# Kernel tuning notes

Measured on AMD Instinct MI355X. Metric: run time of the kernel, lower is better.

Reference implementation:

```python
import jax, jax.numpy as jnp
import numpy as np

B, P, L1, D = 64, 16, 16, 1024  # images, people/img, object slots/img (slot0=no-object), feat dim
SP = 32   # flattened spatial (Conv_spatial output channels)
PROJ = 512
ACT = 29


def setup_inputs() -> dict:
    key = jax.random.key(0)
    ks = jax.random.split(key, 16)
    rn = lambda k, s, sc=1.0: jax.random.normal(k, s, dtype=jnp.float32) * sc
    w = 0.02  # weight init scale
    return {
        "people": rn(ks[0], (B, P, D)),
        "objects": rn(ks[1], (B, L1, D)),
        "context": rn(ks[2], (B, D)),
        "spatial": rn(ks[3], (B, P * L1, SP)),
        "Wvis_w": rn(ks[4], (3 * D, PROJ), w), "Wvis_b": jnp.zeros((PROJ,), jnp.float32),
        "Wspat_w": rn(ks[5], (SP, PROJ), w), "Wspat_b": jnp.zeros((PROJ,), jnp.float32),
        "Wip_w": rn(ks[6], (PROJ, 1), w), "Wip_b": jnp.zeros((1,), jnp.float32),
        "Wref_w": rn(ks[7], (PROJ, ACT), w), "Wref_b": jnp.zeros((ACT,), jnp.float32),
        "Watt_w": rn(ks[8], (PROJ, ACT), w), "Watt_b": jnp.zeros((ACT,), jnp.float32),
        "Woh_w": rn(ks[9], (D, D), w), "Woh_b": jnp.zeros((D,), jnp.float32),
        "Who_w": rn(ks[10], (D, D), w), "Who_b": jnp.zeros((D,), jnp.float32),
        "Wg_w": rn(ks[11], (2 * D, ACT), w), "Wg_b": jnp.zeros((ACT,), jnp.float32),
    }


def reference(people, objects, context, spatial,
              Wvis_w, Wvis_b, Wspat_w, Wspat_b, Wip_w, Wip_b,
              Wref_w, Wref_b, Watt_w, Watt_b,
              Woh_w, Woh_b, Who_w, Who_b, Wg_w, Wg_b):
    Bn, Pn, Dn = people.shape
    L = objects.shape[1]
    C = Bn * Pn * L

    # --- ROI.pairing: all (person, object-slot) pairs + image context -> [C, 3D]
    pe = jnp.broadcast_to(people[:, :, None, :], (Bn, Pn, L, Dn))
    ob = jnp.broadcast_to(objects[:, None, :, :], (Bn, Pn, L, Dn))
    cx = jnp.broadcast_to(context[:, None, None, :], (Bn, Pn, L, Dn))
    pairs = jnp.concatenate([pe, ob, cx], axis=-1).reshape(C, 3 * Dn)

    # --- attention / visual projection heads
    a_ho = jax.nn.relu(spatial.reshape(C, -1) @ Wspat_w + Wspat_b)   # W_Spat
    f_vis = jax.nn.relu(pairs @ Wvis_w + Wvis_b)                     # W_vis
    f_ref = f_vis * a_ho
    i_ho = f_ref @ Wip_w + Wip_b                                     # [C,1]
    interaction_prob = jax.nn.sigmoid(i_ho)
    p_ref = f_ref @ Wref_w + Wref_b                                  # [C,29]
    p_att = a_ho @ Watt_w + Watt_b                                   # [C,29]

    # --- graph message passing: adjacency = interaction probs, skipping slot 0 (no-object)
    adj = interaction_prob.reshape(Bn, Pn, L)[:, :, 1:]              # [B,P,O]
    oh = jax.nn.relu(objects[:, 1:] @ Woh_w + Woh_b)                 # W_oh on objects
    ho = jax.nn.relu(people @ Who_w + Who_b)                         # W_ho on people
    people_r = people + jnp.einsum('bpo,bod->bpd', adj, oh)
    objects_r = objects[:, 1:] + jnp.einsum('bpo,bpd->bod', adj, ho)
    objects_full = jnp.concatenate([objects[:, :1], objects_r], axis=1)  # re-attach no-object slot

    # --- refined all-pairs concat -> W_graph
    pe_r = jnp.broadcast_to(people_r[:, :, None, :], (Bn, Pn, L, Dn))
    ob_r = jnp.broadcast_to(objects_full[:, None, :, :], (Bn, Pn, L, Dn))
    pairs_g = jnp.concatenate([pe_r, ob_r], axis=-1).reshape(C, 2 * Dn)
    p_graph = pairs_g @ Wg_w + Wg_b                                  # [C,29]

    return (i_ho, p_ref, p_att, p_graph)
```

## Files before the change

kernel.cpp:

```cpp
#include <hip/hip_runtime.h>


typedef unsigned short u16;
typedef short s16x8 __attribute__((ext_vector_type(8)));
typedef float f32x4 __attribute__((ext_vector_type(4)));

__device__ __forceinline__ u16 f2b(float f) {
    union { float f; unsigned int i; } v; v.f = f;
    unsigned int r = (v.i + 0x7fffu + ((v.i >> 16) & 1u)) >> 16;
    return (u16)r;
}
__device__ __forceinline__ float b2f(u16 u) {
    union { float f; unsigned int i; } v; v.i = ((unsigned int)u) << 16; return v.f;
}
__device__ __forceinline__ unsigned int pack2(float x, float y) {
    return (unsigned int)f2b(x) | ((unsigned int)f2b(y) << 16);
}

#define OFF_WSPATT 0u
#define OFF_WREFT  32768u
#define OFF_WATTT  65536u
#define OFF_WGT    98304u
#define OFF_PP     229376u
#define OFF_PO     1277952u
#define OFF_PC     2326528u
#define OFF_ADJ    2392064u
#define OFF_HP     2457600u
#define OFF_HOF    2588672u
#define OFF_YH     2719744u
#define OFF_ZO     2850816u
#define ZERO_OFF   2457600u
#define ZERO_LEN   516096u
#define OFF_WVIST2 2973696u
#define OFF_WHOT2  6119424u
#define OFF_WOHT2  8216576u
#define OFF_PEOB   10313728u
#define OFF_OBJB   12410880u
#define OFF_CTXB   14508032u
#define OFF_SPATB  14639104u

__global__ __launch_bounds__(256) void prep_all(
    const float* __restrict__ people, const float* __restrict__ objects,
    const float* __restrict__ context, const float* __restrict__ spatial,
    const float* __restrict__ Wvis, const float* __restrict__ Who,
    const float* __restrict__ Woh, const float* __restrict__ Wspat,
    const float* __restrict__ Wref, const float* __restrict__ Watt,
    const float* __restrict__ Wg,
    u16* __restrict__ peoB, u16* __restrict__ objB, u16* __restrict__ ctxB,
    u16* __restrict__ spatB, u16* __restrict__ WvisT, u16* __restrict__ WhoT,
    u16* __restrict__ WohT, u16* __restrict__ WspatT, u16* __restrict__ WrefT,
    u16* __restrict__ WattT, u16* __restrict__ WgT, float* __restrict__ zeroWS)
{
    __shared__ float S[64][65];
    int bid = blockIdx.x, t = threadIdx.x;
    if (bid < 896) {
        const float* src; u16* dst; int N, K, kt, nt;
        int tb = bid;
        if (tb < 256)      { src = Who;  dst = WhoT;  K = 1024; N = 1024; kt = tb >> 4; nt = tb & 15; }
        else if (tb < 512) { tb -= 256; src = Woh;  dst = WohT;  K = 1024; N = 1024; kt = tb >> 4; nt = tb & 15; }
        else               { tb -= 512; src = Wvis; dst = WvisT; K = 3072; N = 512;  kt = tb >> 3; nt = tb & 7; }
        int k0 = kt * 64, n0 = nt * 64;
        int r = t >> 4, c4 = (t & 15) * 4;
#pragma unroll
        for (int i = 0; i < 4; i++) {
            float4 v = *(const float4*)&src[(size_t)(k0 + r + 16 * i) * N + n0 + c4];
            S[r + 16 * i][c4 + 0] = v.x;
            S[r + 16 * i][c4 + 1] = v.y;
            S[r + 16 * i][c4 + 2] = v.z;
            S[r + 16 * i][c4 + 3] = v.w;
        }
        __syncthreads();
#pragma unroll
        for (int i = 0; i < 4; i++) {
            int nn = r + 16 * i;
            unsigned int lo = pack2(S[c4 + 0][nn], S[c4 + 1][nn]);
            unsigned int hi = pack2(S[c4 + 2][nn], S[c4 + 3][nn]);
            *(uint2*)&dst[(size_t)(n0 + nn) * K + k0 + c4] = make_uint2(lo, hi);
        }
        return;
    }
    int g = (bid - 896) * 256 + t;
    const int gsz = 512 * 256;
    for (int i = g; i < 262144; i += gsz) {
        float4 v = ((const float4*)people)[i];
        ((uint2*)peoB)[i] = make_uint2(pack2(v.x, v.y), pack2(v.z, v.w));
    }
    for (int i = g; i < 262144; i += gsz) {
        float4 v = ((const float4*)objects)[i];
        ((uint2*)objB)[i] = make_uint2(pack2(v.x, v.y), pack2(v.z, v.w));
    }
    for (int i = g; i < 16384; i += gsz) {
        float4 v = ((const float4*)context)[i];
        ((uint2*)ctxB)[i] = make_uint2(pack2(v.x, v.y), pack2(v.z, v.w));
    }
    for (int i = g; i < 131072; i += gsz) {
        float4 v = ((const float4*)spatial)[i];
        ((uint2*)spatB)[i] = make_uint2(pack2(v.x, v.y), pack2(v.z, v.w));
    }
    for (int i = g; i < 32256; i += gsz) {
        f32x4 z = {0.f, 0.f, 0.f, 0.f};
        ((f32x4*)zeroWS)[i] = z;
    }
    for (int i = g; i < 512 * 32; i += gsz) {
        int n = i >> 5, k = i & 31;
        WspatT[i] = f2b(Wspat[k * 512 + n]);
    }
    for (int i = g; i < 32 * 512; i += gsz) {
        int n = i >> 9, k = i & 511;
        WrefT[i] = (n < 29) ? f2b(Wref[k * 29 + n]) : (u16)0;
        WattT[i] = (n < 29) ? f2b(Watt[k * 29 + n]) : (u16)0;
    }
    for (int i = g; i < 32 * 2048; i += gsz) {
        int n = i >> 11, k = i & 2047;
        WgT[i] = (n < 29) ? f2b(Wg[k * 29 + n]) : (u16)0;
    }
}

__global__ __launch_bounds__(256) void fused_gemms(
    const u16* __restrict__ peoB, const u16* __restrict__ objB,
    const u16* __restrict__ ctxB, const u16* __restrict__ WvisT,
    const u16* __restrict__ WhoT, const float* __restrict__ Who_b,
    const u16* __restrict__ WohT, const float* __restrict__ Woh_b,
    const u16* __restrict__ WgT,
    u16* __restrict__ Pp, u16* __restrict__ Po, u16* __restrict__ Pc,
    float* __restrict__ Yh, float* __restrict__ Zo,
    float* __restrict__ Hp, float* __restrict__ HoF)
{
    __shared__ __align__(16) u16 As[2][64][72];
    __shared__ __align__(16) u16 Bs[2][64][72];

    int b0 = blockIdx.x, bid;
    if (b0 < 264)      bid = (b0 & 7) * 33 + (b0 >> 3);
    else if (b0 < 760) { int l = b0 - 264; bid = 264 + (l & 7) * 62 + (l >> 3); }
    else               { int l = b0 - 760; bid = 760 + (l & 7) * 16 + (l >> 3); }
    int t = threadIdx.x;
    int lane = t & 63, w = t >> 6;
    int l16 = lane & 15, q = lane >> 4;
    int wy = w >> 1, wx = w & 1;

    if (bid < 760) {
        const u16 *Ap, *Bp;
        int Bstride, bm, bn, koff = 0, zrm = 0;
        u16* outB = nullptr;
        const float* bb = nullptr; const u16* Wg2 = nullptr; float* U = nullptr;
        if (bid < 264) {
            int bx = bid & 7, ty = bid >> 3;
            if (ty < 16)      { Ap = peoB; outB = Pp; koff = 0;    bm = ty * 64; }
            else if (ty < 32) { Ap = objB; outB = Po; koff = 1024; bm = (ty - 16) * 64; }
            else              { Ap = ctxB; outB = Pc; koff = 2048; bm = 0; }
            bn = bx * 64;
            Bp = WvisT; Bstride = 3072;
        } else {
            int r3 = bid - 264;
            int zz, rt, nbt;
            if (r3 < 256) { zz = 0; rt = r3 >> 4; nbt = r3 & 15; }
            else          { zz = 1; r3 -= 256; rt = r3 >> 4; nbt = r3 & 15; }
            zrm = zz;
            Ap = zz ? objB : peoB;
            Bp = zz ? WohT : WhoT; Bstride = 1024;
            bb = zz ? Woh_b : Who_b;
            Wg2 = zz ? WgT : WgT + 1024;
            U = zz ? Zo : Yh;
            bm = rt * 64; bn = nbt * 64;
        }

        int tr = t >> 3, tc = (t & 7) * 8;
        int a0r = bm + tr, a1r = bm + 32 + tr;
        if (zrm) { a0r = (a0r / 15) * 16 + (a0r % 15) + 1;
                   a1r = (a1r / 15) * 16 + (a1r % 15) + 1; }
        const u16* gA0 = Ap + (size_t)a0r * 1024 + tc;
        const u16* gA1 = Ap + (size_t)a1r * 1024 + tc;
        const u16* gB0 = Bp + (size_t)(bn + tr) * Bstride + koff + tc;
        const u16* gB1 = Bp + (size_t)(bn + 32 + tr) * Bstride + koff + tc;

        s16x8 rA0 = *(const s16x8*)gA0, rA1 = *(const s16x8*)gA1;
        s16x8 rB0 = *(const s16x8*)gB0, rB1 = *(const s16x8*)gB1;
        gA0 += 64; gA1 += 64; gB0 += 64; gB1 += 64;
        *(s16x8*)&As[0][tr][tc]      = rA0;
        *(s16x8*)&As[0][32 + tr][tc] = rA1;
        *(s16x8*)&Bs[0][tr][tc]      = rB0;
        *(s16x8*)&Bs[0][32 + tr][tc] = rB1;
        rA0 = *(const s16x8*)gA0; rA1 = *(const s16x8*)gA1;
        rB0 = *(const s16x8*)gB0; rB1 = *(const s16x8*)gB1;
        gA0 += 64; gA1 += 64; gB0 += 64; gB1 += 64;
        __syncthreads();

        f32x4 acc00 = {0,0,0,0}, acc01 = {0,0,0,0}, acc10 = {0,0,0,0}, acc11 = {0,0,0,0};
        int cur = 0;
        for (int kt = 0; kt < 16; kt++) {
#pragma unroll
            for (int kk = 0; kk < 2; kk++) {
                s16x8 a0 = *(const s16x8*)&As[cur][wy * 32 + l16][kk * 32 + q * 8];
                s16x8 a1 = *(const s16x8*)&As[cur][wy * 32 + 16 + l16][kk * 32 + q * 8];
                s16x8 b0 = *(const s16x8*)&Bs[cur][wx * 32 + l16][kk * 32 + q * 8];
                s16x8 b1 = *(const s16x8*)&Bs[cur][wx * 32 + 16 + l16][kk * 32 + q * 8];
                acc00 = __builtin_amdgcn_mfma_f32_16x16x32_bf16(a0, b0, acc00, 0, 0, 0);
                acc01 = __builtin_amdgcn_mfma_f32_16x16x32_bf16(a0, b1, acc01, 0, 0, 0);
                acc10 = __builtin_amdgcn_mfma_f32_16x16x32_bf16(a1, b0, acc10, 0, 0, 0);
                acc11 = __builtin_amdgcn_mfma_f32_16x16x32_bf16(a1, b1, acc11, 0, 0, 0);
            }
            if (kt < 15) {
                __syncthreads();
                *(s16x8*)&As[cur ^ 1][tr][tc]      = rA0;
                *(s16x8*)&As[cur ^ 1][32 + tr][tc] = rA1;
                *(s16x8*)&Bs[cur ^ 1][tr][tc]      = rB0;
                *(s16x8*)&Bs[cur ^ 1][32 + tr][tc] = rB1;
                if (kt < 14) {
                    rA0 = *(const s16x8*)gA0; rA1 = *(const s16x8*)gA1;
                    rB0 = *(const s16x8*)gB0; rB1 = *(const s16x8*)gB1;
                    gA0 += 64; gA1 += 64; gB0 += 64; gB1 += 64;
                }
                __syncthreads();
                cur ^= 1;
            }
        }

        f32x4 accs[2][2] = {{acc00, acc01}, {acc10, acc11}};
        if (bid < 264) {
#pragma unroll
            for (int ii = 0; ii < 2; ii++)
#pragma unroll
                for (int jj = 0; jj < 2; jj++) {
                    int col = bn + wx * 32 + jj * 16 + l16;
#pragma unroll
                    for (int r = 0; r < 4; r++) {
                        int row = bm + wy * 32 + ii * 16 + q * 4 + r;
                        outB[(size_t)row * 512 + col] = f2b(accs[ii][jj][r]);
                    }
                }
        } else {
            u16 (*T)[72] = As[0];
#pragma unroll
            for (int ii = 0; ii < 2; ii++)
#pragma unroll
                for (int jj = 0; jj < 2; jj++) {
                    int col = wx * 32 + jj * 16 + l16;
                    float bv = bb[bn + col];
#pragma unroll
                    for (int rr = 0; rr < 4; rr++) {
                        float v = accs[ii][jj][rr] + bv;
                        T[wy * 32 + ii * 16 + q * 4 + rr][col] = f2b(fmaxf(v, 0.f));
                    }
                }
            __syncthreads();

            f32x4 s20 = {0,0,0,0}, s21 = {0,0,0,0};
#pragma unroll
            for (int kk = 0; kk < 64; kk += 32) {
                s16x8 a2 = *(const s16x8*)(&T[w * 16 + l16][kk + q * 8]);
                s16x8 b20 = *(const s16x8*)(Wg2 + (size_t)l16 * 2048 + bn + kk + q * 8);
                s16x8 b21 = *(const s16x8*)(Wg2 + (size_t)(16 + l16) * 2048 + bn + kk + q * 8);
                s20 = __builtin_amdgcn_mfma_f32_16x16x32_bf16(a2, b20, s20, 0, 0, 0);
                s21 = __builtin_amdgcn_mfma_f32_16x16x32_bf16(a2, b21, s21, 0, 0, 0);
            }
#pragma unroll
            for (int rr = 0; rr < 4; rr++) {
                int row = bm + w * 16 + q * 4 + rr;
                atomicAdd(&U[(size_t)row * 32 + l16], s20[rr]);
                atomicAdd(&U[(size_t)row * 32 + 16 + l16], s21[rr]);
            }
        }
    } else {
        int r3 = bid - 760;
        int bx = r3 & 7, by = (r3 >> 3) & 7, z = r3 >> 6;
        const u16* A  = z ? objB : peoB;
        const u16* BT = z ? WgT + 1024 : WgT;
        float* outF   = z ? HoF : Hp;
        int bm = bx * 128 + w * 32;
        int kb = by * 128;
        const u16* ap0 = A + (size_t)(bm + l16) * 1024 + kb + q * 8;
        const u16* ap1 = A + (size_t)(bm + 16 + l16) * 1024 + kb + q * 8;
        const u16* bp0 = BT + (size_t)l16 * 2048 + kb + q * 8;
        const u16* bp1 = BT + (size_t)(16 + l16) * 2048 + kb + q * 8;
        f32x4 acc00 = {0,0,0,0}, acc01 = {0,0,0,0}, acc10 = {0,0,0,0}, acc11 = {0,0,0,0};
        s16x8 bA0[4], bA1[4], bB0[4], bB1[4];
#pragma unroll
        for (int s = 0; s < 4; s++) {
            bA0[s] = *(const s16x8*)(ap0 + s * 32);
            bA1[s] = *(const s16x8*)(ap1 + s * 32);
            bB0[s] = *(const s16x8*)(bp0 + s * 32);
            bB1[s] = *(const s16x8*)(bp1 + s * 32);
        }
#pragma unroll
        for (int s = 0; s < 4; s++) {
            acc00 = __builtin_amdgcn_mfma_f32_16x16x32_bf16(bA0[s], bB0[s], acc00, 0, 0, 0);
            acc01 = __builtin_amdgcn_mfma_f32_16x16x32_bf16(bA0[s], bB1[s], acc01, 0, 0, 0);
            acc10 = __builtin_amdgcn_mfma_f32_16x16x32_bf16(bA1[s], bB0[s], acc10, 0, 0, 0);
            acc11 = __builtin_amdgcn_mfma_f32_16x16x32_bf16(bA1[s], bB1[s], acc11, 0, 0, 0);
        }
        f32x4 accs[2][2] = {{acc00, acc01}, {acc10, acc11}};
#pragma unroll
        for (int ii = 0; ii < 2; ii++)
#pragma unroll
            for (int jj = 0; jj < 2; jj++)
#pragma unroll
                for (int r = 0; r < 4; r++)
                    atomicAdd(&outF[(size_t)(bm + ii * 16 + q * 4 + r) * 32 + jj * 16 + l16],
                              accs[ii][jj][r]);
    }
}

__global__ __launch_bounds__(256) void mega(
    const u16* __restrict__ spatB, const u16* __restrict__ WspatT,
    const float* __restrict__ bspat,
    const u16* __restrict__ Pp, const u16* __restrict__ Po,
    const u16* __restrict__ Pc, const float* __restrict__ bvis,
    const u16* __restrict__ WrefT, const float* __restrict__ bref,
    const u16* __restrict__ WattT, const float* __restrict__ batt,
    const float* __restrict__ wip, const float* __restrict__ bip,
    float* __restrict__ outI, float* __restrict__ outRef,
    float* __restrict__ outAtt, float* __restrict__ adjw)
{
    __shared__ u16 tile[32][512];
    __shared__ float part[32][8];
    __shared__ float wipS[512];
    int t = threadIdx.x;
    int b0 = blockIdx.x;
    int bid = (b0 & 7) * 64 + (b0 >> 3);
    int c0 = bid * 32;
    int lane = t & 63, w = t >> 6;
    int l16 = lane & 15, q = lane >> 4;

    {
        float2 u = *(const float2*)(wip + t * 2);
        wipS[t * 2]     = u.x;
        wipS[t * 2 + 1] = u.y;
    }

    {
        s16x8 a0 = *(const s16x8*)(spatB + (size_t)(c0 + l16) * 32 + q * 8);
        s16x8 a1 = *(const s16x8*)(spatB + (size_t)(c0 + 16 + l16) * 32 + q * 8);
        const u16* wb = WspatT + (size_t)(w * 128 + l16) * 32 + q * 8;
        s16x8 cb = *(const s16x8*)wb;
        s16x8 nb_ = *(const s16x8*)(wb + 16 * 32);
        wb += 32 * 32;
#pragma unroll
        for (int nt = 0; nt < 8; nt++) {
            s16x8 tb;
            if (nt < 6) { tb = *(const s16x8*)wb; wb += 16 * 32; }
            int n = w * 128 + nt * 16;
            f32x4 acc0 = {0,0,0,0}, acc1 = {0,0,0,0};
            acc0 = __builtin_amdgcn_mfma_f32_16x16x32_bf16(a0, cb, acc0, 0, 0, 0);
            acc1 = __builtin_amdgcn_mfma_f32_16x16x32_bf16(a1, cb, acc1, 0, 0, 0);
            cb = nb_; nb_ = tb;
            float bias = bspat[n + l16];
#pragma unroll
            for (int r = 0; r < 4; r++) {
                tile[q * 4 + r][n + l16]      = f2b(fmaxf(acc0[r] + bias, 0.f));
                tile[16 + q * 4 + r][n + l16] = f2b(fmaxf(acc1[r] + bias, 0.f));
            }
        }
    }
    __syncthreads();

    {
        int rt = w >> 1, ct = w & 1;
        const u16* bp = WattT + (size_t)(ct * 16 + l16) * 512 + q * 8;
        const u16* ar = &tile[rt * 16 + l16][q * 8];
        f32x4 acc0 = {0,0,0,0}, acc1 = {0,0,0,0}, acc2 = {0,0,0,0}, acc3 = {0,0,0,0};
#pragma unroll
        for (int s = 0; s < 16; s += 4) {
            s16x8 a0 = *(const s16x8*)(ar + (s + 0) * 32);
            s16x8 a1 = *(const s16x8*)(ar + (s + 1) * 32);
            s16x8 a2 = *(const s16x8*)(ar + (s + 2) * 32);
            s16x8 a3 = *(const s16x8*)(ar + (s + 3) * 32);
            s16x8 b0 = *(const s16x8*)(bp + (s + 0) * 32);
            s16x8 b1 = *(const s16x8*)(bp + (s + 1) * 32);
            s16x8 b2 = *(const s16x8*)(bp + (s + 2) * 32);
            s16x8 b3 = *(const s16x8*)(bp + (s + 3) * 32);
            acc0 = __builtin_amdgcn_mfma_f32_16x16x32_bf16(a0, b0, acc0, 0, 0, 0);
            acc1 = __builtin_amdgcn_mfma_f32_16x16x32_bf16(a1, b1, acc1, 0, 0, 0);
            acc2 = __builtin_amdgcn_mfma_f32_16x16x32_bf16(a2, b2, acc2, 0, 0, 0);
            acc3 = __builtin_amdgcn_mfma_f32_16x16x32_bf16(a3, b3, acc3, 0, 0, 0);
        }
        f32x4 acc = (acc0 + acc1) + (acc2 + acc3);
        int col = ct * 16 + l16;
        if (col < 29) {
            float bias = batt[col];
#pragma unroll
            for (int r = 0; r < 4; r++) {
                int row = c0 + rt * 16 + q * 4 + r;
                outAtt[(size_t)row * 29 + col] = acc[r] + bias;
            }
        }
    }
    __syncthreads();

    {
        int row = t >> 3, g = t & 7;
        int c = c0 + row;
        int rp = c >> 4, bimg = c >> 8;
        int ro = bimg * 16 + (c & 15);
        const u16* ppr = Pp + (size_t)rp * 512;
        const u16* por = Po + (size_t)ro * 512;
        const u16* pcr = Pc + (size_t)bimg * 512;
        float ps = 0.f;
#pragma unroll 4
        for (int j = 0; j < 64; j += 2) {
            int col = g * 64 + j;
            unsigned int upp = *(const unsigned int*)(ppr + col);
            unsigned int upo = *(const unsigned int*)(por + col);
            unsigned int upc = *(const unsigned int*)(pcr + col);
            float2 bv = *(const float2*)(bvis + col);
            unsigned int uah = *(const unsigned int*)(&tile[row][col]);
            float fv0 = fmaxf(b2f((u16)(upp & 0xffff)) + b2f((u16)(upo & 0xffff))
                            + b2f((u16)(upc & 0xffff)) + bv.x, 0.f);
            float fv1 = fmaxf(b2f((u16)(upp >> 16)) + b2f((u16)(upo >> 16))
                            + b2f((u16)(upc >> 16)) + bv.y, 0.f);
            float fr0 = fv0 * b2f((u16)(uah & 0xffff));
            float fr1 = fv1 * b2f((u16)(uah >> 16));
            *(unsigned int*)(&tile[row][col]) = pack2(fr0, fr1);
            ps += fr0 * wipS[col] + fr1 * wipS[col + 1];
        }
        part[row][g] = ps;
    }
    __syncthreads();

    if (t < 32) {
        float s = part[t][0] + part[t][1] + part[t][2] + part[t][3]
                + part[t][4] + part[t][5] + part[t][6] + part[t][7] + bip[0];
        outI[c0 + t] = s;
        adjw[c0 + t] = 1.f / (1.f + expf(-s));
    }

    {
        int rt = w >> 1, ct = w & 1;
        const u16* bp = WrefT + (size_t)(ct * 16 + l16) * 512 + q * 8;
        const u16* ar = &tile[rt * 16 + l16][q * 8];
        f32x4 acc0 = {0,0,0,0}, acc1 = {0,0,0,0}, acc2 = {0,0,0,0}, acc3 = {0,0,0,0};
#pragma unroll
        for (int s = 0; s < 16; s += 4) {
            s16x8 a0 = *(const s16x8*)(ar + (s + 0) * 32);
            s16x8 a1 = *(const s16x8*)(ar + (s + 1) * 32);
            s16x8 a2 = *(const s16x8*)(ar + (s + 2) * 32);
            s16x8 a3 = *(const s16x8*)(ar + (s + 3) * 32);
            s16x8 b0 = *(const s16x8*)(bp + (s + 0) * 32);
            s16x8 b1 = *(const s16x8*)(bp + (s + 1) * 32);
            s16x8 b2 = *(const s16x8*)(bp + (s + 2) * 32);
            s16x8 b3 = *(const s16x8*)(bp + (s + 3) * 32);
            acc0 = __builtin_amdgcn_mfma_f32_16x16x32_bf16(a0, b0, acc0, 0, 0, 0);
            acc1 = __builtin_amdgcn_mfma_f32_16x16x32_bf16(a1, b1, acc1, 0, 0, 0);
            acc2 = __builtin_amdgcn_mfma_f32_16x16x32_bf16(a2, b2, acc2, 0, 0, 0);
            acc3 = __builtin_amdgcn_mfma_f32_16x16x32_bf16(a3, b3, acc3, 0, 0, 0);
        }
        f32x4 acc = (acc0 + acc1) + (acc2 + acc3);
        int col = ct * 16 + l16;
        if (col < 29) {
            float bias = bref[col];
#pragma unroll
            for (int r = 0; r < 4; r++) {
                int row = c0 + rt * 16 + q * 4 + r;
                outRef[(size_t)row * 29 + col] = acc[r] + bias;
            }
        }
    }
}

__global__ __launch_bounds__(256) void pgraph2(
    const float* __restrict__ adjw, const float* __restrict__ Hp,
    const float* __restrict__ HoF, const float* __restrict__ Yh,
    const float* __restrict__ Zo, const float* __restrict__ bg,
    float* __restrict__ outG)
{
    int b = blockIdx.x, t = threadIdx.x;
    __shared__ float adjS[16][16];
    __shared__ float YhS[16][32];
    __shared__ float ZoS[15][32];
    __shared__ float PA[16][32];
    __shared__ float OA[16][32];
    adjS[t >> 4][t & 15] = adjw[b * 256 + t];
    for (int i = t; i < 512; i += 256)
        YhS[i >> 5][i & 31] = Yh[(size_t)(b * 16 + (i >> 5)) * 32 + (i & 31)];
    for (int i = t; i < 480; i += 256)
        ZoS[i >> 5][i & 31] = Zo[(size_t)(b * 15 + (i >> 5)) * 32 + (i & 31)];
    __syncthreads();
    for (int i = t; i < 512; i += 256) {
        int p = i >> 5, j = i & 31;
        float s = 0.f;
#pragma unroll
        for (int o = 0; o < 15; o++) s += adjS[p][o + 1] * ZoS[o][j];
        PA[p][j] = s;
        float s2 = 0.f;
#pragma unroll
        for (int pp = 0; pp < 16; pp++) s2 += adjS[pp][p] * YhS[pp][j];
        OA[p][j] = s2;
    }
    __syncthreads();
    int p = t >> 4, l = t & 15;
    const float* hp = Hp + (size_t)(b * 16 + p) * 32;
    const float* ho = HoF + (size_t)(b * 16 + l) * 32;
    size_t c = (size_t)b * 256 + t;
    for (int j = 0; j < 29; j++) {
        float v = hp[j] + ho[j] + bg[j] + PA[p][j];
        if (l >= 1) v += OA[l][j];
        outG[c * 29 + j] = v;
    }
}

extern "C" void kernel_launch(void* const* d_in, const int* in_sizes, int n_in,
                              void* d_out, int out_size, void* d_ws, size_t ws_size,
                              hipStream_t stream)
{
    const float* people  = (const float*)d_in[0];
    const float* objects = (const float*)d_in[1];
    const float* context = (const float*)d_in[2];
    const float* spatial = (const float*)d_in[3];
    const float* Wvis_w  = (const float*)d_in[4];
    const float* Wvis_b  = (const float*)d_in[5];
    const float* Wspat_w = (const float*)d_in[6];
    const float* Wspat_b = (const float*)d_in[7];
    const float* Wip_w   = (const float*)d_in[8];
    const float* Wip_b   = (const float*)d_in[9];
    const float* Wref_w  = (const float*)d_in[10];
    const float* Wref_b  = (const float*)d_in[11];
    const float* Watt_w  = (const float*)d_in[12];
    const float* Watt_b  = (const float*)d_in[13];
    const float* Woh_w   = (const float*)d_in[14];
    const float* Woh_b   = (const float*)d_in[15];
    const float* Who_w   = (const float*)d_in[16];
    const float* Who_b   = (const float*)d_in[17];
    const float* Wg_w    = (const float*)d_in[18];
    const float* Wg_b    = (const float*)d_in[19];

    char* ws = (char*)d_ws;
    u16* WspatT = (u16*)(ws + OFF_WSPATT);
    u16* WrefT  = (u16*)(ws + OFF_WREFT);
    u16* WattT  = (u16*)(ws + OFF_WATTT);
    u16* WgT    = (u16*)(ws + OFF_WGT);
    u16* Ppb    = (u16*)(ws + OFF_PP);
    u16* Pob    = (u16*)(ws + OFF_PO);
    u16* Pcb    = (u16*)(ws + OFF_PC);
    float* adjw = (float*)(ws + OFF_ADJ);
    float* Hp   = (float*)(ws + OFF_HP);
    float* HoF  = (float*)(ws + OFF_HOF);
    float* Yh   = (float*)(ws + OFF_YH);
    float* Zo   = (float*)(ws + OFF_ZO);
    u16* WvisT2 = (u16*)(ws + OFF_WVIST2);
    u16* WhoT2  = (u16*)(ws + OFF_WHOT2);
    u16* WohT2  = (u16*)(ws + OFF_WOHT2);
    u16* peoB   = (u16*)(ws + OFF_PEOB);
    u16* objB   = (u16*)(ws + OFF_OBJB);
    u16* ctxB   = (u16*)(ws + OFF_CTXB);
    u16* spatB  = (u16*)(ws + OFF_SPATB);
    float* zeroWS = (float*)(ws + ZERO_OFF);

    float* outI   = (float*)d_out;
    float* outRef = outI + 16384;
    float* outAtt = outI + 491520;
    float* outG   = outI + 966656;

    prep_all<<<1408, 256, 0, stream>>>(people, objects, context, spatial,
        Wvis_w, Who_w, Woh_w, Wspat_w, Wref_w, Watt_w, Wg_w,
        peoB, objB, ctxB, spatB, WvisT2, WhoT2, WohT2,
        WspatT, WrefT, WattT, WgT, zeroWS);

    fused_gemms<<<888, 256, 0, stream>>>(peoB, objB, ctxB, WvisT2,
        WhoT2, Who_b, WohT2, Woh_b, WgT,
        Ppb, Pob, Pcb, Yh, Zo, Hp, HoF);

    mega<<<512, 256, 0, stream>>>(spatB, WspatT, Wspat_b,
                                  Ppb, Pob, Pcb, Wvis_b,
                                  WrefT, Wref_b, WattT, Watt_b,
                                  Wip_w, Wip_b,
                                  outI, outRef, outAtt, adjw);

    pgraph2<<<64, 256, 0, stream>>>(adjw, Hp, HoF, Yh, Zo, Wg_b, outG);
}
```

Baseline: 155.6 us.

## Move spatial projection and attention head into fused_gemms as extra blocks

The W_spat projection (a_ho) and the p_att head move out of the mega kernel into 512 extra blocks of fused_gemms, which run alongside the visual and graph GEMM blocks. The a_ho tile is written to a new bf16 workspace buffer, and mega now reads it from global memory instead of computing it into shared memory. This shortens mega's critical path and fills otherwise idle GPU slots in fused_gemms. The cost is an extra global round-trip of about 16 MB of bf16 a_ho data and a larger fused_gemms grid.

```diff
diff --git a/kernel.cpp b/kernel.cpp
--- a/kernel.cpp
+++ b/kernel.cpp
@@ -38,6 +38,7 @@
 #define OFF_OBJB   12410880u
 #define OFF_CTXB   14508032u
 #define OFF_SPATB  14639104u
+#define OFF_AHOB   15687680u
 
 __global__ __launch_bounds__(256) void prep_all(
     const float* __restrict__ people, const float* __restrict__ objects,
@@ -122,17 +123,23 @@
     const u16* __restrict__ WhoT, const float* __restrict__ Who_b,
     const u16* __restrict__ WohT, const float* __restrict__ Woh_b,
     const u16* __restrict__ WgT,
+    const u16* __restrict__ spatB, const u16* __restrict__ WspatT,
+    const float* __restrict__ bspat,
+    const u16* __restrict__ WattT, const float* __restrict__ batt,
     u16* __restrict__ Pp, u16* __restrict__ Po, u16* __restrict__ Pc,
     float* __restrict__ Yh, float* __restrict__ Zo,
-    float* __restrict__ Hp, float* __restrict__ HoF)
+    float* __restrict__ Hp, float* __restrict__ HoF,
+    u16* __restrict__ ahoB, float* __restrict__ outAtt)
 {
-    __shared__ __align__(16) u16 As[2][64][72];
-    __shared__ __align__(16) u16 Bs[2][64][72];
+    __shared__ __align__(16) unsigned char LB[36864];
+    u16 (*As)[64][72] = (u16(*)[64][72])LB;
+    u16 (*Bs)[64][72] = (u16(*)[64][72])(LB + 18432);
 
     int b0 = blockIdx.x, bid;
     if (b0 < 264)      bid = (b0 & 7) * 33 + (b0 >> 3);
     else if (b0 < 760) { int l = b0 - 264; bid = 264 + (l & 7) * 62 + (l >> 3); }
-    else               { int l = b0 - 760; bid = 760 + (l & 7) * 16 + (l >> 3); }
+    else if (b0 < 888) { int l = b0 - 760; bid = 760 + (l & 7) * 16 + (l >> 3); }
+    else               { int l = b0 - 888; bid = 888 + (l & 7) * 64 + (l >> 3); }
     int t = threadIdx.x;
     int lane = t & 63, w = t >> 6;
     int l16 = lane & 15, q = lane >> 4;
@@ -260,7 +267,7 @@
                 atomicAdd(&U[(size_t)row * 32 + 16 + l16], s21[rr]);
             }
         }
-    } else {
+    } else if (bid < 888) {
         int r3 = bid - 760;
         int bx = r3 & 7, by = (r3 >> 3) & 7, z = r3 >> 6;
         const u16* A  = z ? objB : peoB;
@@ -297,19 +304,84 @@
                 for (int r = 0; r < 4; r++)
                     atomicAdd(&outF[(size_t)(bm + ii * 16 + q * 4 + r) * 32 + jj * 16 + l16],
                               accs[ii][jj][r]);
+    } else {
+        u16 (*tile)[512] = (u16(*)[512])LB;
+        int c0 = (bid - 888) * 32;
+
+        {
+            s16x8 a0 = *(const s16x8*)(spatB + (size_t)(c0 + l16) * 32 + q * 8);
+            s16x8 a1 = *(const s16x8*)(spatB + (size_t)(c0 + 16 + l16) * 32 + q * 8);
+            const u16* wb = WspatT + (size_t)(w * 128 + l16) * 32 + q * 8;
+            s16x8 cb = *(const s16x8*)wb;
+            s16x8 nb_ = *(const s16x8*)(wb + 16 * 32);
+            wb += 32 * 32;
+#pragma unroll
+            for (int nt = 0; nt < 8; nt++) {
+                s16x8 tb;
+                if (nt < 6) { tb = *(const s16x8*)wb; wb += 16 * 32; }
+                int n = w * 128 + nt * 16;
+                f32x4 acc0 = {0,0,0,0}, acc1 = {0,0,0,0};
+                acc0 = __builtin_amdgcn_mfma_f32_16x16x32_bf16(a0, cb, acc0, 0, 0, 0);
+                acc1 = __builtin_amdgcn_mfma_f32_16x16x32_bf16(a1, cb, acc1, 0, 0, 0);
+                cb = nb_; nb_ = tb;
+                float bias = bspat[n + l16];
+#pragma unroll
+                for (int r = 0; r < 4; r++) {
+                    tile[q * 4 + r][n + l16]      = f2b(fmaxf(acc0[r] + bias, 0.f));
+                    tile[16 + q * 4 + r][n + l16] = f2b(fmaxf(acc1[r] + bias, 0.f));
+                }
+            }
+        }
+        __syncthreads();
+
+        {
+            int rt = w >> 1, ct = w & 1;
+            const u16* bp = WattT + (size_t)(ct * 16 + l16) * 512 + q * 8;
+            const u16* ar = &tile[rt * 16 + l16][q * 8];
+            f32x4 acc0 = {0,0,0,0}, acc1 = {0,0,0,0}, acc2 = {0,0,0,0}, acc3 = {0,0,0,0};
+#pragma unroll
+            for (int s = 0; s < 16; s += 4) {
+                s16x8 a0 = *(const s16x8*)(ar + (s + 0) * 32);
+                s16x8 a1 = *(const s16x8*)(ar + (s + 1) * 32);
+                s16x8 a2 = *(const s16x8*)(ar + (s + 2) * 32);
+                s16x8 a3 = *(const s16x8*)(ar + (s + 3) * 32);
+                s16x8 b0 = *(const s16x8*)(bp + (s + 0) * 32);
+                s16x8 b1 = *(const s16x8*)(bp + (s + 1) * 32);
+                s16x8 b2 = *(const s16x8*)(bp + (s + 2) * 32);
+                s16x8 b3 = *(const s16x8*)(bp + (s + 3) * 32);
+                acc0 = __builtin_amdgcn_mfma_f32_16x16x32_bf16(a0, b0, acc0, 0, 0, 0);
+                acc1 = __builtin_amdgcn_mfma_f32_16x16x32_bf16(a1, b1, acc1, 0, 0, 0);
+                acc2 = __builtin_amdgcn_mfma_f32_16x16x32_bf16(a2, b2, acc2, 0, 0, 0);
+                acc3 = __builtin_amdgcn_mfma_f32_16x16x32_bf16(a3, b3, acc3, 0, 0, 0);
+            }
+            f32x4 acc = (acc0 + acc1) + (acc2 + acc3);
+            int col = ct * 16 + l16;
+            if (col < 29) {
+                float bias = batt[col];
+#pragma unroll
+                for (int r = 0; r < 4; r++) {
+                    int row = c0 + rt * 16 + q * 4 + r;
+                    outAtt[(size_t)row * 29 + col] = acc[r] + bias;
+                }
+            }
+        }
+
+        {
+            const uint4* ts = (const uint4*)tile;
+            uint4* gd = (uint4*)(ahoB + (size_t)c0 * 512);
+            for (int i = t; i < 2048; i += 256) gd[i] = ts[i];
+        }
     }
 }
 
 __global__ __launch_bounds__(256) void mega(
-    const u16* __restrict__ spatB, const u16* __restrict__ WspatT,
-    const float* __restrict__ bspat,
+    const u16* __restrict__ ahoB,
     const u16* __restrict__ Pp, const u16* __restrict__ Po,
     const u16* __restrict__ Pc, const float* __restrict__ bvis,
     const u16* __restrict__ WrefT, const float* __restrict__ bref,
-    const u16* __restrict__ WattT, const float* __restrict__ batt,
     const float* __restrict__ wip, const float* __restrict__ bip,
     float* __restrict__ outI, float* __restrict__ outRef,
-    float* __restrict__ outAtt, float* __restrict__ adjw)
+    float* __restrict__ adjw)
 {
     __shared__ u16 tile[32][512];
     __shared__ float part[32][8];
@@ -326,64 +398,6 @@
         wipS[t * 2]     = u.x;
         wipS[t * 2 + 1] = u.y;
     }
-
-    {
-        s16x8 a0 = *(const s16x8*)(spatB + (size_t)(c0 + l16) * 32 + q * 8);
-        s16x8 a1 = *(const s16x8*)(spatB + (size_t)(c0 + 16 + l16) * 32 + q * 8);
-        const u16* wb = WspatT + (size_t)(w * 128 + l16) * 32 + q * 8;
-        s16x8 cb = *(const s16x8*)wb;
-        s16x8 nb_ = *(const s16x8*)(wb + 16 * 32);
-        wb += 32 * 32;
-#pragma unroll
-        for (int nt = 0; nt < 8; nt++) {
-            s16x8 tb;
-            if (nt < 6) { tb = *(const s16x8*)wb; wb += 16 * 32; }
-            int n = w * 128 + nt * 16;
-            f32x4 acc0 = {0,0,0,0}, acc1 = {0,0,0,0};
-            acc0 = __builtin_amdgcn_mfma_f32_16x16x32_bf16(a0, cb, acc0, 0, 0, 0);
-            acc1 = __builtin_amdgcn_mfma_f32_16x16x32_bf16(a1, cb, acc1, 0, 0, 0);
-            cb = nb_; nb_ = tb;
-            float bias = bspat[n + l16];
-#pragma unroll
-            for (int r = 0; r < 4; r++) {
-                tile[q * 4 + r][n + l16]      = f2b(fmaxf(acc0[r] + bias, 0.f));
-                tile[16 + q * 4 + r][n + l16] = f2b(fmaxf(acc1[r] + bias, 0.f));
-            }
-        }
-    }
-    __syncthreads();
-
-    {
-        int rt = w >> 1, ct = w & 1;
-        const u16* bp = WattT + (size_t)(ct * 16 + l16) * 512 + q * 8;
-        const u16* ar = &tile[rt * 16 + l16][q * 8];
-        f32x4 acc0 = {0,0,0,0}, acc1 = {0,0,0,0}, acc2 = {0,0,0,0}, acc3 = {0,0,0,0};
-#pragma unroll
-        for (int s = 0; s < 16; s += 4) {
-            s16x8 a0 = *(const s16x8*)(ar + (s + 0) * 32);
-            s16x8 a1 = *(const s16x8*)(ar + (s + 1) * 32);
-            s16x8 a2 = *(const s16x8*)(ar + (s + 2) * 32);
-            s16x8 a3 = *(const s16x8*)(ar + (s + 3) * 32);
-            s16x8 b0 = *(const s16x8*)(bp + (s + 0) * 32);
-            s16x8 b1 = *(const s16x8*)(bp + (s + 1) * 32);
-            s16x8 b2 = *(const s16x8*)(bp + (s + 2) * 32);
-            s16x8 b3 = *(const s16x8*)(bp + (s + 3) * 32);
-            acc0 = __builtin_amdgcn_mfma_f32_16x16x32_bf16(a0, b0, acc0, 0, 0, 0);
-            acc1 = __builtin_amdgcn_mfma_f32_16x16x32_bf16(a1, b1, acc1, 0, 0, 0);
-            acc2 = __builtin_amdgcn_mfma_f32_16x16x32_bf16(a2, b2, acc2, 0, 0, 0);
-            acc3 = __builtin_amdgcn_mfma_f32_16x16x32_bf16(a3, b3, acc3, 0, 0, 0);
-        }
-        f32x4 acc = (acc0 + acc1) + (acc2 + acc3);
-        int col = ct * 16 + l16;
-        if (col < 29) {
-            float bias = batt[col];
-#pragma unroll
-            for (int r = 0; r < 4; r++) {
-                int row = c0 + rt * 16 + q * 4 + r;
-                outAtt[(size_t)row * 29 + col] = acc[r] + bias;
-            }
-        }
-    }
     __syncthreads();
 
     {
@@ -394,6 +408,7 @@
         const u16* ppr = Pp + (size_t)rp * 512;
         const u16* por = Po + (size_t)ro * 512;
         const u16* pcr = Pc + (size_t)bimg * 512;
+        const u16* ahr = ahoB + (size_t)c * 512;
         float ps = 0.f;
 #pragma unroll 4
         for (int j = 0; j < 64; j += 2) {
@@ -402,7 +417,7 @@
             unsigned int upo = *(const unsigned int*)(por + col);
             unsigned int upc = *(const unsigned int*)(pcr + col);
             float2 bv = *(const float2*)(bvis + col);
-            unsigned int uah = *(const unsigned int*)(&tile[row][col]);
+            unsigned int uah = *(const unsigned int*)(ahr + col);
             float fv0 = fmaxf(b2f((u16)(upp & 0xffff)) + b2f((u16)(upo & 0xffff))
                             + b2f((u16)(upc & 0xffff)) + bv.x, 0.f);
             float fv1 = fmaxf(b2f((u16)(upp >> 16)) + b2f((u16)(upo >> 16))
@@ -542,6 +557,7 @@
     u16* objB   = (u16*)(ws + OFF_OBJB);
     u16* ctxB   = (u16*)(ws + OFF_CTXB);
     u16* spatB  = (u16*)(ws + OFF_SPATB);
+    u16* ahoB   = (u16*)(ws + OFF_AHOB);
     float* zeroWS = (float*)(ws + ZERO_OFF);
 
     float* outI   = (float*)d_out;
@@ -554,15 +570,17 @@
         peoB, objB, ctxB, spatB, WvisT2, WhoT2, WohT2,
         WspatT, WrefT, WattT, WgT, zeroWS);
 
-    fused_gemms<<<888, 256, 0, stream>>>(peoB, objB, ctxB, WvisT2,
+    fused_gemms<<<1400, 256, 0, stream>>>(peoB, objB, ctxB, WvisT2,
         WhoT2, Who_b, WohT2, Woh_b, WgT,
-        Ppb, Pob, Pcb, Yh, Zo, Hp, HoF);
-
-    mega<<<512, 256, 0, stream>>>(spatB, WspatT, Wspat_b,
+        spatB, WspatT, Wspat_b, WattT, Watt_b,
+        Ppb, Pob, Pcb, Yh, Zo, Hp, HoF,
+        ahoB, outAtt);
+
+    mega<<<512, 256, 0, stream>>>(ahoB,
                                   Ppb, Pob, Pcb, Wvis_b,
-                                  WrefT, Wref_b, WattT, Watt_b,
+                                  WrefT, Wref_b,
                                   Wip_w, Wip_b,
-                                  outI, outRef, outAtt, adjw);
+                                  outI, outRef, adjw);
 
     pgraph2<<<64, 256, 0, stream>>>(adjw, Hp, HoF, Yh, Zo, Wg_b, outG);
 }
```

Result: no change. 156.6 us (+0.7%).
